# Kernel tuning notes

Measured on AMD Instinct MI355X. Metric: run time of the kernel, lower is better.

The kernel has to match this reference:

```python
import jax, jax.numpy as jnp
import numpy as np

CH = 8        # MASK_HEAD.CHANNELS
CIN = 8       # MASK_BRANCH.OUT_CHANNELS
# weight/bias split offsets for 3-layer head with rel coords:
# w0=(CIN+2)*CH=80, w1=CH*CH=64, w2=CH*1=8, b0=8, b1=8, b2=1 -> 169


def _bilinear_align_corners(x, Ho, Wo):
    # x: [n, c, H, W] -> [n, c, Ho, Wo], matches F.interpolate(align_corners=True)
    n, c, H, W = x.shape
    ys = jnp.arange(Ho, dtype=x.dtype) * ((H - 1) / (Ho - 1))
    xs = jnp.arange(Wo, dtype=x.dtype) * ((W - 1) / (Wo - 1))
    y0 = jnp.floor(ys).astype(jnp.int32)
    y1 = jnp.minimum(y0 + 1, H - 1)
    wy = (ys - y0.astype(x.dtype))[:, None]
    x0 = jnp.floor(xs).astype(jnp.int32)
    x1 = jnp.minimum(x0 + 1, W - 1)
    wx = xs - x0.astype(x.dtype)
    rows = x[..., y0, :] * (1.0 - wy) + x[..., y1, :] * wy   # [n,c,Ho,W]
    out = rows[..., x0] * (1.0 - wx) + rows[..., x1] * wx    # [n,c,Ho,Wo]
    return out


def setup_inputs() -> dict:
    key = jax.random.key(0)
    k1, k2, k3, k4, k5, k6 = jax.random.split(key, 6)
    N, H, W = 2, 128, 192
    n_inst = 256
    stride = 8
    mask_feats = jax.random.normal(k1, (N, CIN, H, W), dtype=jnp.float32)
    mask_head_params = jax.random.normal(k2, (n_inst, 169), dtype=jnp.float32) * 0.1
    # instance center locations in image coords (stride-8 feature covers [0, W*stride))
    instance_locations = jax.random.uniform(k3, (n_inst, 2), dtype=jnp.float32) * jnp.array(
        [W * stride, H * stride], dtype=jnp.float32
    )
    fpn_levels = jax.random.randint(k4, (n_inst,), 0, 5, dtype=jnp.int32)
    soi_table = jnp.array([64.0, 128.0, 256.0, 512.0, 1024.0], dtype=jnp.float32)
    sizes_of_interest = soi_table[fpn_levels]  # pre-gathered soi per instance
    im_inds = jax.random.randint(k5, (n_inst,), 0, N, dtype=jnp.int32)
    return {
        "mask_feats": mask_feats,
        "mask_head_params": mask_head_params,
        "instance_locations": instance_locations,
        "sizes_of_interest": sizes_of_interest,
        "im_inds": im_inds,
        "fpn_levels": fpn_levels,
        "mask_feat_stride": 8,
    }


def reference(mask_feats, mask_head_params, instance_locations, sizes_of_interest,
              im_inds, fpn_levels, mask_feat_stride):
    N, _, H, W = mask_feats.shape
    n_inst = mask_head_params.shape[0]
    dt = mask_feats.dtype

    # compute_locations(H, W, stride): (x, y) centers of the mask-feat grid
    shifts_x = jnp.arange(W, dtype=dt) * mask_feat_stride + mask_feat_stride // 2
    shifts_y = jnp.arange(H, dtype=dt) * mask_feat_stride + mask_feat_stride // 2
    xx, yy = jnp.meshgrid(shifts_x, shifts_y)              # [H, W]
    locations = jnp.stack([xx.ravel(), yy.ravel()], axis=1)  # [HW, 2]

    # relative coords per instance, normalized by size-of-interest of its FPN level
    rel = instance_locations[:, None, :] - locations[None, :, :]   # [n, HW, 2]
    rel = jnp.transpose(rel, (0, 2, 1)) / sizes_of_interest[:, None, None]  # [n, 2, HW]

    feats = mask_feats[im_inds].reshape(n_inst, CIN, H * W)        # gather per instance
    x = jnp.concatenate([rel.astype(dt), feats], axis=1).reshape(n_inst, CIN + 2, H, W)

    p = mask_head_params
    w0 = p[:, 0:80].reshape(n_inst, CH, CIN + 2)
    w1 = p[:, 80:144].reshape(n_inst, CH, CH)
    w2 = p[:, 144:152].reshape(n_inst, 1, CH)
    b0 = p[:, 152:160]
    b1 = p[:, 160:168]
    b2 = p[:, 168:169]

    # per-instance 1x1 convs == batched small GEMMs over the spatial grid
    x = jax.nn.relu(jnp.einsum('noc,nchw->nohw', w0, x) + b0[:, :, None, None])
    x = jax.nn.relu(jnp.einsum('noc,nchw->nohw', w1, x) + b1[:, :, None, None])
    x = jnp.einsum('noc,nchw->nohw', w2, x) + b2[:, :, None, None]  # [n,1,H,W]

    # inference path: F.interpolate(scale_factor=2, mode='bilinear', align_corners=True)
    return _bilinear_align_corners(x, 2 * H, 2 * W)
```

## Files before the change

### kernel.cpp

```cpp
#include <hip/hip_runtime.h>

typedef float f32x2 __attribute__((ext_vector_type(2)));
typedef float f32x4 __attribute__((ext_vector_type(4)));
typedef _Float16 h16x2 __attribute__((ext_vector_type(2)));

#define HH 128
#define WW 192
#define HO 256
#define WO 384
#define NINST 256
#define OTY 16
#define LTY 10
#define LPAD 196
#define STRIPS 24
#define PSTRIDE 170
#define WS_NEED (NINST * PSTRIDE * 2)

static __device__ __forceinline__ unsigned pkrtz(float a, float b) {
    return __builtin_bit_cast(unsigned, __builtin_amdgcn_cvt_pkrtz(a, b));
}

static __device__ __forceinline__ float dot2(unsigned a, unsigned b, float c) {
#if __has_builtin(__builtin_amdgcn_fdot2)
    return __builtin_amdgcn_fdot2(__builtin_bit_cast(h16x2, a),
                                  __builtin_bit_cast(h16x2, b), c, false);
#else
    h16x2 x = __builtin_bit_cast(h16x2, a), y = __builtin_bit_cast(h16x2, b);
    return fmaf((float)x[1], (float)y[1], fmaf((float)x[0], (float)y[0], c));
#endif
}

__global__ __launch_bounds__(256) void prep_params(const float* __restrict__ p,
                                                   unsigned short* __restrict__ o16) {
    int j = blockIdx.x * 256 + threadIdx.x;
    if (j < NINST * 169) {
        int n = j / 169, k = j - n * 169;
        _Float16 h = (_Float16)p[j];
        o16[n * PSTRIDE + k] = __builtin_bit_cast(unsigned short, h);
    }
}

__global__ __launch_bounds__(256) void dynmask_fused(
    const float* __restrict__ feats,
    const float* __restrict__ params,
    const unsigned short* __restrict__ params16,
    const float* __restrict__ locs,
    const float* __restrict__ soi,
    const int*   __restrict__ im_inds,
    const int*   __restrict__ stride_p,
    float* __restrict__ out)
{
    const int n   = blockIdx.y;
    const int t   = threadIdx.x;
    const int oy0 = blockIdx.x * OTY;

    __shared__ float tile[LTY][LPAD];

    const float sy = 127.0f / 255.0f;
    const float sx = 191.0f / 383.0f;
    const int ly0 = (int)((float)oy0 * sy);

    const float* __restrict__ pw = params + n * 169;
    const unsigned short* __restrict__ pw16 = params16 + n * PSTRIDE;
    const int   stride  = *stride_p;
    const float inv_soi = 1.0f / soi[n];
    const float loc_x   = locs[2*n+0];
    const float loc_y   = locs[2*n+1];
    const float* fbase  = feats + im_inds[n] * (8*HH*WW);
    const float xstep   = -(float)stride * inv_soi;

    #define W0P(o,kp) (*(const unsigned*)(pw16 + (o)*10 + 2 + 2*(kp)))
    #define W1P(o,kp) (*(const unsigned*)(pw16 + 80 + (o)*8 + 2*(kp)))
    #define W2P(kp)   (*(const unsigned*)(pw16 + 144 + 2*(kp)))

    if (t < LTY * STRIPS) {
        const int r  = (unsigned)t / STRIPS;
        const int c0 = (t - r*STRIPS) * 8;
        int gy = ly0 + r; if (gy > HH-1) gy = HH-1;
        const float* frow = fbase + gy*WW + c0;

        const float yrel = (loc_y - (float)(gy*stride + (stride>>1))) * inv_soi;
        const float xr0  = (loc_x - (float)(c0*stride + (stride>>1))) * inv_soi;

        float wxw[8], byo[8];
        #pragma unroll
        for (int o = 0; o < 8; ++o) {
            wxw[o] = pw[o*10+0];
            byo[o] = fmaf(yrel, pw[o*10+1], pw[152+o]);
        }

        #pragma unroll
        for (int g = 0; g < 2; ++g) {
            f32x4 f[8];
            #pragma unroll
            for (int ch = 0; ch < 8; ++ch)
                f[ch] = *(const f32x4*)(frow + ch*(HH*WW) + g*4);

            float xr[4];
            #pragma unroll
            for (int j = 0; j < 4; ++j)
                xr[j] = fmaf((float)(g*4+j), xstep, xr0);

            unsigned fp[4][4];
            #pragma unroll
            for (int cp = 0; cp < 4; ++cp)
                #pragma unroll
                for (int j = 0; j < 4; ++j)
                    fp[cp][j] = pkrtz(f[2*cp][j], f[2*cp+1][j]);

            float h0[4][8];
            #pragma unroll
            for (int o = 0; o < 8; ++o) {
                #pragma unroll
                for (int j = 0; j < 4; ++j) {
                    float a = fmaf(xr[j], wxw[o], byo[o]);
                    a = dot2(fp[0][j], W0P(o,0), a);
                    a = dot2(fp[1][j], W0P(o,1), a);
                    a = dot2(fp[2][j], W0P(o,2), a);
                    a = dot2(fp[3][j], W0P(o,3), a);
                    h0[j][o] = fmaxf(a, 0.0f);
                }
            }

            unsigned hp[4][4];
            #pragma unroll
            for (int j = 0; j < 4; ++j)
                #pragma unroll
                for (int cp = 0; cp < 4; ++cp)
                    hp[j][cp] = pkrtz(h0[j][2*cp], h0[j][2*cp+1]);

            float h1[4][8];
            #pragma unroll
            for (int o = 0; o < 8; ++o) {
                #pragma unroll
                for (int j = 0; j < 4; ++j) {
                    float a = pw[160+o];
                    a = dot2(hp[j][0], W1P(o,0), a);
                    a = dot2(hp[j][1], W1P(o,1), a);
                    a = dot2(hp[j][2], W1P(o,2), a);
                    a = dot2(hp[j][3], W1P(o,3), a);
                    h1[j][o] = fmaxf(a, 0.0f);
                }
            }

            f32x4 rv;
            #pragma unroll
            for (int j = 0; j < 4; ++j) {
                unsigned p0 = pkrtz(h1[j][0], h1[j][1]);
                unsigned p1 = pkrtz(h1[j][2], h1[j][3]);
                unsigned p2 = pkrtz(h1[j][4], h1[j][5]);
                unsigned p3 = pkrtz(h1[j][6], h1[j][7]);
                float a = pw[168];
                a = dot2(p0, W2P(0), a);
                a = dot2(p1, W2P(1), a);
                a = dot2(p2, W2P(2), a);
                a = dot2(p3, W2P(3), a);
                rv[j] = a;
            }
            *(f32x4*)&tile[r][c0 + g*4] = rv;
        }
    }

    __syncthreads();

    float* obase = out + (size_t)n * (HO*WO);
    #pragma unroll
    for (int k = 0; k < 3; ++k) {
        const int u    = t + k*256;
        const int wrap = (u >= 384);
        const int col  = wrap ? u - 384 : u;
        const int r0o  = wrap ? 8 : 0;

        const float xsf = (float)col * sx;
        int ix0 = (int)xsf; if (ix0 > WW-2) ix0 = WW-2;
        const float wx = xsf - (float)ix0;
        const float* tcol = &tile[0][0] + ix0;

        float a, b, c, d;
        int prevIy = -999;
        float* optr = obase + (size_t)(oy0 + r0o) * WO + col;

        for (int rr = 0; rr < 8; ++rr) {
            const int   yo  = oy0 + r0o + rr;
            const float ysf = (float)yo * sy;
            int iy0 = (int)ysf; if (iy0 > HH-2) iy0 = HH-2;
            const float wy = ysf - (float)iy0;

            if (iy0 != prevIy) {
                const float* p = tcol + (iy0 - ly0) * LPAD;
                if (iy0 == prevIy + 1) {
                    a = c; b = d;
                    c = p[LPAD]; d = p[LPAD+1];
                } else {
                    a = p[0];    b = p[1];
                    c = p[LPAD]; d = p[LPAD+1];
                }
                prevIy = iy0;
            }

            float va = fmaf(wy, c - a, a);
            float vb = fmaf(wy, d - b, b);
            *optr = fmaf(wx, vb - va, va);
            optr += WO;
        }
    }
    #undef W0P
    #undef W1P
    #undef W2P
}

__global__ __launch_bounds__(256) void dynmask_fused_f32(
    const float* __restrict__ feats,
    const float* __restrict__ params,
    const float* __restrict__ locs,
    const float* __restrict__ soi,
    const int*   __restrict__ im_inds,
    const int*   __restrict__ stride_p,
    float* __restrict__ out)
{
    const int n   = blockIdx.y;
    const int t   = threadIdx.x;
    const int oy0 = blockIdx.x * OTY;

    __shared__ float tile[LTY][LPAD];

    const float sy = 127.0f / 255.0f;
    const float sx = 191.0f / 383.0f;
    const int ly0 = (int)((float)oy0 * sy);

    const float* __restrict__ pw = params + n * 169;
    const int   stride  = *stride_p;
    const float inv_soi = 1.0f / soi[n];
    const float loc_x   = locs[2*n+0];
    const float loc_y   = locs[2*n+1];
    const float* fbase  = feats + im_inds[n] * (8*HH*WW);
    const float xstep   = -(float)stride * inv_soi;

    if (t < LTY * STRIPS) {
        const int r  = (unsigned)t / STRIPS;
        const int c0 = (t - r*STRIPS) * 8;
        int gy = ly0 + r; if (gy > HH-1) gy = HH-1;
        const float* frow = fbase + gy*WW + c0;

        const float yrel = (loc_y - (float)(gy*stride + (stride>>1))) * inv_soi;
        const float xr0  = (loc_x - (float)(c0*stride + (stride>>1))) * inv_soi;

        #pragma unroll
        for (int g = 0; g < 2; ++g) {
            f32x4 f[8];
            #pragma unroll
            for (int ch = 0; ch < 8; ++ch)
                f[ch] = *(const f32x4*)(frow + ch*(HH*WW) + g*4);

            float xr[4];
            #pragma unroll
            for (int j = 0; j < 4; ++j)
                xr[j] = fmaf((float)(g*4+j), xstep, xr0);

            float h0[4][8];
            #pragma unroll
            for (int o = 0; o < 8; ++o) {
                const float byo = fmaf(yrel, pw[o*10+1], pw[152+o]);
                const float wxw = pw[o*10+0];
                #pragma unroll
                for (int j = 0; j < 4; ++j) {
                    float a = fmaf(xr[j], wxw, byo);
                    #pragma unroll
                    for (int ch = 0; ch < 8; ++ch)
                        a = fmaf(f[ch][j], pw[o*10+2+ch], a);
                    h0[j][o] = fmaxf(a, 0.0f);
                }
            }

            f32x4 rv;
            #pragma unroll
            for (int j = 0; j < 4; ++j) rv[j] = pw[168];
            #pragma unroll
            for (int o = 0; o < 8; ++o) {
                const float b1w = pw[160+o];
                const float w2w = pw[144+o];
                #pragma unroll
                for (int j = 0; j < 4; ++j) {
                    float a = b1w;
                    #pragma unroll
                    for (int c = 0; c < 8; ++c)
                        a = fmaf(h0[j][c], pw[80+o*8+c], a);
                    rv[j] = fmaf(fmaxf(a, 0.0f), w2w, rv[j]);
                }
            }
            *(f32x4*)&tile[r][c0 + g*4] = rv;
        }
    }

    __syncthreads();

    float* obase = out + (size_t)n * (HO*WO);
    #pragma unroll
    for (int k = 0; k < 3; ++k) {
        const int u    = t + k*256;
        const int wrap = (u >= 384);
        const int col  = wrap ? u - 384 : u;
        const int r0o  = wrap ? 8 : 0;

        const float xsf = (float)col * sx;
        int ix0 = (int)xsf; if (ix0 > WW-2) ix0 = WW-2;
        const float wx = xsf - (float)ix0;
        const float* tcol = &tile[0][0] + ix0;

        float a, b, c, d;
        int prevIy = -999;
        float* optr = obase + (size_t)(oy0 + r0o) * WO + col;

        for (int rr = 0; rr < 8; ++rr) {
            const int   yo  = oy0 + r0o + rr;
            const float ysf = (float)yo * sy;
            int iy0 = (int)ysf; if (iy0 > HH-2) iy0 = HH-2;
            const float wy = ysf - (float)iy0;

            if (iy0 != prevIy) {
                const float* p = tcol + (iy0 - ly0) * LPAD;
                if (iy0 == prevIy + 1) {
                    a = c; b = d;
                    c = p[LPAD]; d = p[LPAD+1];
                } else {
                    a = p[0];    b = p[1];
                    c = p[LPAD]; d = p[LPAD+1];
                }
                prevIy = iy0;
            }

            float va = fmaf(wy, c - a, a);
            float vb = fmaf(wy, d - b, b);
            *optr = fmaf(wx, vb - va, va);
            optr += WO;
        }
    }
}

extern "C" void kernel_launch(void* const* d_in, const int* in_sizes, int n_in,
                              void* d_out, int out_size, void* d_ws, size_t ws_size,
                              hipStream_t stream) {
    const float* feats    = (const float*)d_in[0];
    const float* params   = (const float*)d_in[1];
    const float* locs     = (const float*)d_in[2];
    const float* soi      = (const float*)d_in[3];
    const int*   im_inds  = (const int*)d_in[4];
    const int*   stride_p = (const int*)d_in[6];
    float* out = (float*)d_out;

    dim3 grid(HO / OTY, NINST);
    dim3 block(256);

    if (ws_size >= (size_t)WS_NEED) {
        unsigned short* params16 = (unsigned short*)d_ws;
        hipLaunchKernelGGL(prep_params, dim3(170), dim3(256), 0, stream,
                           params, params16);
        hipLaunchKernelGGL(dynmask_fused, grid, block, 0, stream,
                           feats, params, params16, locs, soi, im_inds, stride_p, out);
    } else {
        hipLaunchKernelGGL(dynmask_fused_f32, grid, block, 0, stream,
                           feats, params, locs, soi, im_inds, stride_p, out);
    }
}
```

Baseline: 54.96 us.

## Transpose features to NHWC, use fp32 FMAs, and enlarge output tile per block

Adds a prep kernel that transposes mask features into an NHWC workspace, so each thread loads a pixel's 8 channels contiguously. The fp16 dot2 path and the param-conversion kernel are replaced with plain fp32 FMAs reading weights directly. Layers 1 and 2 are fused so no intermediate is stored. Blocks grow to 512 threads covering 32 output rows, and only the needed low-res rows are computed. This cuts redundant halo recomputation and per-instance launch overhead, at the cost of more ALU work in fp32 and an extra transpose pass.

```diff
diff --git a/kernel.cpp b/kernel.cpp
--- a/kernel.cpp
+++ b/kernel.cpp
@@ -1,49 +1,36 @@
 #include <hip/hip_runtime.h>
 
-typedef float f32x2 __attribute__((ext_vector_type(2)));
 typedef float f32x4 __attribute__((ext_vector_type(4)));
-typedef _Float16 h16x2 __attribute__((ext_vector_type(2)));
 
 #define HH 128
 #define WW 192
 #define HO 256
 #define WO 384
 #define NINST 256
-#define OTY 16
-#define LTY 10
+#define NPX (HH*WW)
+#define OTY 32
+#define LTY 18
 #define LPAD 196
 #define STRIPS 24
-#define PSTRIDE 170
-#define WS_NEED (NINST * PSTRIDE * 2)
-
-static __device__ __forceinline__ unsigned pkrtz(float a, float b) {
-    return __builtin_bit_cast(unsigned, __builtin_amdgcn_cvt_pkrtz(a, b));
+#define NT 512
+#define WS_NEED (2 * NPX * 8 * 4)
+
+__global__ __launch_bounds__(256) void prep_nhwc(const float* __restrict__ f,
+                                                 float* __restrict__ o) {
+    const int j  = blockIdx.x * 256 + threadIdx.x;
+    const int im = j / NPX;
+    const int p  = j - im * NPX;
+    const float* src = f + im * 8 * NPX + p;
+    f32x4 a, b;
+    a.x = src[0*NPX]; a.y = src[1*NPX]; a.z = src[2*NPX]; a.w = src[3*NPX];
+    b.x = src[4*NPX]; b.y = src[5*NPX]; b.z = src[6*NPX]; b.w = src[7*NPX];
+    *(f32x4*)(o + (size_t)j*8)     = a;
+    *(f32x4*)(o + (size_t)j*8 + 4) = b;
 }
 
-static __device__ __forceinline__ float dot2(unsigned a, unsigned b, float c) {
-#if __has_builtin(__builtin_amdgcn_fdot2)
-    return __builtin_amdgcn_fdot2(__builtin_bit_cast(h16x2, a),
-                                  __builtin_bit_cast(h16x2, b), c, false);
-#else
-    h16x2 x = __builtin_bit_cast(h16x2, a), y = __builtin_bit_cast(h16x2, b);
-    return fmaf((float)x[1], (float)y[1], fmaf((float)x[0], (float)y[0], c));
-#endif
-}
-
-__global__ __launch_bounds__(256) void prep_params(const float* __restrict__ p,
-                                                   unsigned short* __restrict__ o16) {
-    int j = blockIdx.x * 256 + threadIdx.x;
-    if (j < NINST * 169) {
-        int n = j / 169, k = j - n * 169;
-        _Float16 h = (_Float16)p[j];
-        o16[n * PSTRIDE + k] = __builtin_bit_cast(unsigned short, h);
-    }
-}
-
-__global__ __launch_bounds__(256) void dynmask_fused(
-    const float* __restrict__ feats,
+__global__ __launch_bounds__(NT) void dynmask_fused(
+    const float* __restrict__ featsT,
     const float* __restrict__ params,
-    const unsigned short* __restrict__ params16,
     const float* __restrict__ locs,
     const float* __restrict__ soi,
     const int*   __restrict__ im_inds,
@@ -58,104 +45,79 @@
 
     const float sy = 127.0f / 255.0f;
     const float sx = 191.0f / 383.0f;
-    const int ly0 = (int)((float)oy0 * sy);
+
+    const int ly0    = (int)((float)oy0 * sy);
+    int lylast       = (int)((float)(oy0 + OTY - 1) * sy) + 1;
+    if (lylast > HH - 1) lylast = HH - 1;
+    const int lcount = lylast - ly0 + 1;
 
     const float* __restrict__ pw = params + n * 169;
-    const unsigned short* __restrict__ pw16 = params16 + n * PSTRIDE;
     const int   stride  = *stride_p;
     const float inv_soi = 1.0f / soi[n];
     const float loc_x   = locs[2*n+0];
     const float loc_y   = locs[2*n+1];
-    const float* fbase  = feats + im_inds[n] * (8*HH*WW);
+    const float* fbaseT = featsT + (size_t)im_inds[n] * (NPX * 8);
     const float xstep   = -(float)stride * inv_soi;
 
-    #define W0P(o,kp) (*(const unsigned*)(pw16 + (o)*10 + 2 + 2*(kp)))
-    #define W1P(o,kp) (*(const unsigned*)(pw16 + 80 + (o)*8 + 2*(kp)))
-    #define W2P(kp)   (*(const unsigned*)(pw16 + 144 + 2*(kp)))
-
-    if (t < LTY * STRIPS) {
+    const int nstrips = lcount * STRIPS;
+    if (t < nstrips) {
         const int r  = (unsigned)t / STRIPS;
         const int c0 = (t - r*STRIPS) * 8;
-        int gy = ly0 + r; if (gy > HH-1) gy = HH-1;
-        const float* frow = fbase + gy*WW + c0;
+        const int gy = ly0 + r;
+        const float* base = fbaseT + ((size_t)gy * WW + c0) * 8;
 
         const float yrel = (loc_y - (float)(gy*stride + (stride>>1))) * inv_soi;
         const float xr0  = (loc_x - (float)(c0*stride + (stride>>1))) * inv_soi;
 
-        float wxw[8], byo[8];
+        float byo[8];
         #pragma unroll
-        for (int o = 0; o < 8; ++o) {
-            wxw[o] = pw[o*10+0];
+        for (int o = 0; o < 8; ++o)
             byo[o] = fmaf(yrel, pw[o*10+1], pw[152+o]);
-        }
 
         #pragma unroll
         for (int g = 0; g < 2; ++g) {
-            f32x4 f[8];
-            #pragma unroll
-            for (int ch = 0; ch < 8; ++ch)
-                f[ch] = *(const f32x4*)(frow + ch*(HH*WW) + g*4);
+            f32x4 L[8];
+            #pragma unroll
+            for (int k = 0; k < 8; ++k)
+                L[k] = *(const f32x4*)(base + g*32 + k*4);
 
             float xr[4];
             #pragma unroll
             for (int j = 0; j < 4; ++j)
                 xr[j] = fmaf((float)(g*4+j), xstep, xr0);
 
-            unsigned fp[4][4];
-            #pragma unroll
-            for (int cp = 0; cp < 4; ++cp)
-                #pragma unroll
-                for (int j = 0; j < 4; ++j)
-                    fp[cp][j] = pkrtz(f[2*cp][j], f[2*cp+1][j]);
-
             float h0[4][8];
             #pragma unroll
             for (int o = 0; o < 8; ++o) {
+                const float wxw = pw[o*10+0];
                 #pragma unroll
                 for (int j = 0; j < 4; ++j) {
-                    float a = fmaf(xr[j], wxw[o], byo[o]);
-                    a = dot2(fp[0][j], W0P(o,0), a);
-                    a = dot2(fp[1][j], W0P(o,1), a);
-                    a = dot2(fp[2][j], W0P(o,2), a);
-                    a = dot2(fp[3][j], W0P(o,3), a);
+                    float a = fmaf(xr[j], wxw, byo[o]);
+                    #pragma unroll
+                    for (int c = 0; c < 4; ++c)
+                        a = fmaf(L[2*j][c], pw[o*10+2+c], a);
+                    #pragma unroll
+                    for (int c = 0; c < 4; ++c)
+                        a = fmaf(L[2*j+1][c], pw[o*10+6+c], a);
                     h0[j][o] = fmaxf(a, 0.0f);
                 }
             }
 
-            unsigned hp[4][4];
-            #pragma unroll
-            for (int j = 0; j < 4; ++j)
-                #pragma unroll
-                for (int cp = 0; cp < 4; ++cp)
-                    hp[j][cp] = pkrtz(h0[j][2*cp], h0[j][2*cp+1]);
-
-            float h1[4][8];
+            f32x4 rv;
+            #pragma unroll
+            for (int j = 0; j < 4; ++j) rv[j] = pw[168];
             #pragma unroll
             for (int o = 0; o < 8; ++o) {
+                const float b1w = pw[160+o];
+                const float w2w = pw[144+o];
                 #pragma unroll
                 for (int j = 0; j < 4; ++j) {
-                    float a = pw[160+o];
-                    a = dot2(hp[j][0], W1P(o,0), a);
-                    a = dot2(hp[j][1], W1P(o,1), a);
-                    a = dot2(hp[j][2], W1P(o,2), a);
-                    a = dot2(hp[j][3], W1P(o,3), a);
-                    h1[j][o] = fmaxf(a, 0.0f);
-                }
-            }
-
-            f32x4 rv;
-            #pragma unroll
-            for (int j = 0; j < 4; ++j) {
-                unsigned p0 = pkrtz(h1[j][0], h1[j][1]);
-                unsigned p1 = pkrtz(h1[j][2], h1[j][3]);
-                unsigned p2 = pkrtz(h1[j][4], h1[j][5]);
-                unsigned p3 = pkrtz(h1[j][6], h1[j][7]);
-                float a = pw[168];
-                a = dot2(p0, W2P(0), a);
-                a = dot2(p1, W2P(1), a);
-                a = dot2(p2, W2P(2), a);
-                a = dot2(p3, W2P(3), a);
-                rv[j] = a;
+                    float a = b1w;
+                    #pragma unroll
+                    for (int c = 0; c < 8; ++c)
+                        a = fmaf(h0[j][c], pw[80+o*8+c], a);
+                    rv[j] = fmaf(fmaxf(a, 0.0f), w2w, rv[j]);
+                }
             }
             *(f32x4*)&tile[r][c0 + g*4] = rv;
         }
@@ -166,10 +128,10 @@
     float* obase = out + (size_t)n * (HO*WO);
     #pragma unroll
     for (int k = 0; k < 3; ++k) {
-        const int u    = t + k*256;
-        const int wrap = (u >= 384);
-        const int col  = wrap ? u - 384 : u;
-        const int r0o  = wrap ? 8 : 0;
+        const int u   = t + k*NT;
+        const int rg  = (unsigned)u / 384u;
+        const int col = u - rg*384;
+        const int r0o = rg * 8;
 
         const float xsf = (float)col * sx;
         int ix0 = (int)xsf; if (ix0 > WW-2) ix0 = WW-2;
@@ -204,9 +166,6 @@
             optr += WO;
         }
     }
-    #undef W0P
-    #undef W1P
-    #undef W2P
 }
 
 __global__ __launch_bounds__(256) void dynmask_fused_f32(
@@ -220,9 +179,9 @@
 {
     const int n   = blockIdx.y;
     const int t   = threadIdx.x;
-    const int oy0 = blockIdx.x * OTY;
-
-    __shared__ float tile[LTY][LPAD];
+    const int oy0 = blockIdx.x * 16;
+
+    __shared__ float tile[10][LPAD];
 
     const float sy = 127.0f / 255.0f;
     const float sx = 191.0f / 383.0f;
@@ -236,7 +195,7 @@
     const float* fbase  = feats + im_inds[n] * (8*HH*WW);
     const float xstep   = -(float)stride * inv_soi;
 
-    if (t < LTY * STRIPS) {
+    if (t < 10 * STRIPS) {
         const int r  = (unsigned)t / STRIPS;
         const int c0 = (t - r*STRIPS) * 8;
         int gy = ly0 + r; if (gy > HH-1) gy = HH-1;
@@ -348,17 +307,16 @@
     const int*   stride_p = (const int*)d_in[6];
     float* out = (float*)d_out;
 
-    dim3 grid(HO / OTY, NINST);
-    dim3 block(256);
-
     if (ws_size >= (size_t)WS_NEED) {
-        unsigned short* params16 = (unsigned short*)d_ws;
-        hipLaunchKernelGGL(prep_params, dim3(170), dim3(256), 0, stream,
-                           params, params16);
-        hipLaunchKernelGGL(dynmask_fused, grid, block, 0, stream,
-                           feats, params, params16, locs, soi, im_inds, stride_p, out);
+        float* featsT = (float*)d_ws;
+        hipLaunchKernelGGL(prep_nhwc, dim3(2*NPX/256), dim3(256), 0, stream,
+                           feats, featsT);
+        dim3 grid(HO / OTY, NINST);
+        hipLaunchKernelGGL(dynmask_fused, grid, dim3(NT), 0, stream,
+                           featsT, params, locs, soi, im_inds, stride_p, out);
     } else {
-        hipLaunchKernelGGL(dynmask_fused_f32, grid, block, 0, stream,
+        dim3 grid(HO / 16, NINST);
+        hipLaunchKernelGGL(dynmask_fused_f32, grid, dim3(256), 0, stream,
                            feats, params, locs, soi, im_inds, stride_p, out);
     }
 }
```

Measured after the change: 63.97 us. +16.4%, slower.
